# Performance work log

Hardware: AMD Instinct MI355X
Metric: run time of the kernel (lower is better)

## Reference

```python
import jax, jax.numpy as jnp
import numpy as np

NHEAD = 8
HEAD_DIM = 64
WIN = 16  # attention_window w


def _window_index(T, w):
    # For shift slot i in [0, 2w], window[i, t] corresponds to source index t + (i - w).
    W = 2 * w + 1
    j = jnp.arange(T)[None, :] + (jnp.arange(W) - w)[:, None]  # [W, T]
    valid = (j >= 0) & (j < T)
    return jnp.clip(j, 0, T - 1), valid


def setup_inputs() -> dict:
    key = jax.random.key(0)
    ks = jax.random.split(key, 8)
    B, T, N, E = 2, 256, 8, 512
    scale = 1.0 / np.sqrt(E).astype(np.float32)
    return {
        "query": jax.random.normal(ks[0], (B, T, N, E), jnp.float32),
        "key": jax.random.normal(ks[1], (B, T, N, E), jnp.float32),
        "value": jax.random.normal(ks[2], (B, T, N, E), jnp.float32),
        "key_padding_mask": jnp.zeros((B, T, N), dtype=bool),
        "Wq": jax.random.normal(ks[3], (E, E), jnp.float32) * scale,
        "bq": jnp.zeros((E,), jnp.float32),
        "Wk": jax.random.normal(ks[4], (E, E), jnp.float32) * scale,
        "bk": jnp.zeros((E,), jnp.float32),
        "Wv": jax.random.normal(ks[5], (E, E), jnp.float32) * scale,
        "bv": jnp.zeros((E,), jnp.float32),
    }


def reference(query, key, value, key_padding_mask, Wq, bq, Wk, bk, Wv, bv):
    B, T, N, E = query.shape
    h, d, w = NHEAD, HEAD_DIM, WIN
    W = 2 * w + 1
    # linear projections (torch nn.Linear: x @ W.T + b)
    q = (query @ Wq.T + bq).reshape(B, T, N, h, d) / np.float32(np.sqrt(d))
    k = (key @ Wk.T + bk).reshape(B, T, N, h, d)
    v = (value @ Wv.T + bv).reshape(B, T, N, h, d)

    jc, valid = _window_index(T, w)           # [W, T], [W, T]
    vmask6 = valid[None, :, :, None, None, None]
    kwin = jnp.where(vmask6, k[:, jc], 0.0)   # [B, W, T, N, h, d]
    vwin = jnp.where(vmask6, v[:, jc], 0.0)   # [B, W, T, N, h, d]
    # mask: True = masked out (out-of-range stays True, like generate_mask)
    mwin = jnp.where(valid[None, :, :, None], key_padding_mask[:, jc], True)  # [B, W, T, N]

    logits = jnp.einsum('btnhd,bwtmhd->btnwmh', q, kwin)  # [B,T,N,W,N,h]
    mask = mwin.transpose(0, 2, 1, 3)[:, :, None, :, :, None]  # [B,T,1,W,N,1]
    logits = jnp.where(mask, -jnp.inf, logits)

    attn = jax.nn.softmax(logits.reshape(B, T, N, W * N, h), axis=-2)

    vw = vwin.transpose(0, 2, 1, 3, 4, 5).reshape(B, T, W * N, h, d)
    out = jnp.einsum('btnmh,btmhd->btnhd', attn, vw).reshape(B, T, N, E)
    return out, attn
```

## Files before the change

### kernel.cpp

```cpp
#include <hip/hip_runtime.h>
#include <hip/hip_bf16.h>

#define TSEQ 256
#define NBATCH 2
#define NAG 8
#define NH 8
#define HD 64
#define EE 512
#define WHALF 16
#define WW 33
#define WN 264

typedef __attribute__((ext_vector_type(8))) short short8;
typedef __attribute__((ext_vector_type(4))) short short4v;
typedef __attribute__((ext_vector_type(4))) float f32x4;
typedef _Float16 f16x8 __attribute__((ext_vector_type(8)));

static __device__ __forceinline__ unsigned short f2bf(float f) {
    unsigned int u = __float_as_uint(f);
    unsigned int r = (u + 0x7FFFu + ((u >> 16) & 1u)) >> 16;
    return (unsigned short)r;
}
static __device__ __forceinline__ unsigned int cvt_pk_bf16(float lo, float hi) {
    unsigned int r;
    asm("v_cvt_pk_bf16_f32 %0, %1, %2" : "=v"(r) : "v"(lo), "v"(hi));
    return r;
}
static __device__ __forceinline__ unsigned short f2h(float f) {
    _Float16 h = (_Float16)f;
    return __builtin_bit_cast(unsigned short, h);
}
static __device__ __forceinline__ float h2f(unsigned short u) {
    return (float)__builtin_bit_cast(_Float16, u);
}
static __device__ __forceinline__ f16x8 as_f16x8(short8 s) {
    return __builtin_bit_cast(f16x8, s);
}

__global__ __launch_bounds__(256)
void proj_mfma_kernel(const float* __restrict__ xq, const float* __restrict__ xk,
                      const float* __restrict__ xv,
                      const float* __restrict__ Wq, const float* __restrict__ Wk,
                      const float* __restrict__ Wv,
                      const float* __restrict__ bq, const float* __restrict__ bk,
                      const float* __restrict__ bv,
                      unsigned short* __restrict__ oq,
                      unsigned short* __restrict__ kswz,
                      unsigned short* __restrict__ vswz)
{
    __shared__ __align__(16) char LS[24576];
    char* As = LS;
    char* Bs = LS + 8192;

    const float* x; const float* W; const float* bias; float scale;
    const int z = blockIdx.z;
    if (z == 0)      { x = xq; W = Wq; bias = bq; scale = 0.125f; }
    else if (z == 1) { x = xk; W = Wk; bias = bk; scale = 1.0f; }
    else             { x = xv; W = Wv; bias = bv; scale = 1.0f; }

    const int tid  = threadIdx.x;
    const int lane = tid & 63;
    const int wid  = tid >> 6;
    const int i0 = blockIdx.x * 64;
    const int f0 = blockIdx.y * 128;
    const int wr = wid >> 1, wc = wid & 1;

    f32x4 acc[2][4];
    #pragma unroll
    for (int m = 0; m < 2; ++m)
        #pragma unroll
        for (int n = 0; n < 4; ++n)
            acc[m][n] = (f32x4){0.f, 0.f, 0.f, 0.f};

    for (int k0 = 0; k0 < EE; k0 += 64) {
        #pragma unroll
        for (int it = 0; it < 4; ++it) {
            const int tt  = tid + it * 256;
            const int row = tt >> 4, f4 = tt & 15;
            float4 v4 = *reinterpret_cast<const float4*>(x + (size_t)(i0 + row) * EE + k0 + f4 * 4);
            uint2 u;
            u.x = cvt_pk_bf16(v4.x, v4.y);
            u.y = cvt_pk_bf16(v4.z, v4.w);
            *(uint2*)(As + row * 128 + ((f4 * 8) ^ ((row & 7) << 4))) = u;
        }
        #pragma unroll
        for (int it = 0; it < 8; ++it) {
            const int tt  = tid + it * 256;
            const int row = tt >> 4, f4 = tt & 15;
            float4 v4 = *reinterpret_cast<const float4*>(W + (size_t)(f0 + row) * EE + k0 + f4 * 4);
            uint2 u;
            u.x = cvt_pk_bf16(v4.x, v4.y);
            u.y = cvt_pk_bf16(v4.z, v4.w);
            *(uint2*)(Bs + row * 128 + ((f4 * 8) ^ ((row & 7) << 4))) = u;
        }
        __syncthreads();

        #pragma unroll
        for (int ks = 0; ks < 2; ++ks) {
            short8 a[2], b[4];
            #pragma unroll
            for (int m = 0; m < 2; ++m) {
                const int row = wr * 32 + m * 16 + (lane & 15);
                a[m] = *(short8*)(As + row * 128 +
                                  ((ks * 64 + (lane >> 4) * 16) ^ ((row & 7) << 4)));
            }
            #pragma unroll
            for (int n = 0; n < 4; ++n) {
                const int row = wc * 64 + n * 16 + (lane & 15);
                b[n] = *(short8*)(Bs + row * 128 +
                                  ((ks * 64 + (lane >> 4) * 16) ^ ((row & 7) << 4)));
            }
            #pragma unroll
            for (int m = 0; m < 2; ++m)
                #pragma unroll
                for (int n = 0; n < 4; ++n)
                    acc[m][n] = __builtin_amdgcn_mfma_f32_16x16x32_bf16(a[m], b[n], acc[m][n], 0, 0, 0);
        }
        __syncthreads();
    }

    if (z == 0) {
        #pragma unroll
        for (int n = 0; n < 4; ++n) {
            const int col = f0 + wc * 64 + n * 16 + (lane & 15);
            const float bb = bias[col];
            #pragma unroll
            for (int m = 0; m < 2; ++m)
                #pragma unroll
                for (int rg = 0; rg < 4; ++rg) {
                    const int row = i0 + wr * 32 + m * 16 + (lane >> 4) * 4 + rg;
                    oq[(size_t)row * EE + col] = f2bf((acc[m][n][rg] + bb) * scale);
                }
        }
    } else if (z == 1) {
        unsigned short* ls16 = (unsigned short*)LS;
        const int b_ = i0 >> 11;
        const int c0 = i0 & 2047;
        const int h0 = f0 >> 6;
        #pragma unroll
        for (int n = 0; n < 4; ++n) {
            const int col = f0 + wc * 64 + n * 16 + (lane & 15);
            const int hl = (col >> 6) & 1;
            const int d  = col & 63;
            const float bb = bias[col];
            const int ib = (d >> 5) * 512 + ((d & 31) >> 3) * 128 + (d & 7);
            #pragma unroll
            for (int m = 0; m < 2; ++m) {
                #pragma unroll
                for (int rg = 0; rg < 4; ++rg) {
                    const int cl = wr * 32 + m * 16 + (lane >> 4) * 4 + rg;
                    ls16[(hl * 4 + (cl >> 4)) * 1024 + ib + (cl & 15) * 8] =
                        f2bf(acc[m][n][rg] + bb);
                }
            }
        }
        __syncthreads();
        #pragma unroll
        for (int it = 0; it < 4; ++it) {
            const int ci = tid + it * 256;
            const int hlfg = ci >> 7;
            const int hl = hlfg >> 2, fg = hlfg & 3;
            short8 v = *(short8*)(ls16 + ci * 8);
            *(short8*)(kswz + (size_t)(b_ * 8 + h0 + hl) * 131072 +
                       (size_t)((c0 >> 4) + fg) * 1024 + (ci & 127) * 8) = v;
        }
    } else {
        unsigned short* ls16 = (unsigned short*)LS;
        const int b_ = i0 >> 11;
        const int c0 = i0 & 2047;
        const int h0 = f0 >> 6;
        #pragma unroll
        for (int n = 0; n < 4; ++n) {
            const int col = f0 + wc * 64 + n * 16 + (lane & 15);
            const int hl = (col >> 6) & 1;
            const int d  = col & 63;
            const float bb = bias[col];
            const int ib = (d >> 4) * 512 + (d & 15) * 8;
            #pragma unroll
            for (int m = 0; m < 2; ++m) {
                #pragma unroll
                for (int rg = 0; rg < 4; ++rg) {
                    const int cl = wr * 32 + m * 16 + (lane >> 4) * 4 + rg;
                    ls16[(hl * 2 + (cl >> 5)) * 2048 + ib + ((cl >> 3) & 3) * 128 + (cl & 7)] =
                        f2h(acc[m][n][rg] + bb);
                }
            }
        }
        __syncthreads();
        #pragma unroll
        for (int it = 0; it < 4; ++it) {
            const int ci = tid + it * 256;
            const int hlch = ci >> 8;
            const int hl = hlch >> 1, ch = hlch & 1;
            short8 v = *(short8*)(ls16 + ci * 8);
            *(short8*)(vswz + (size_t)(b_ * 8 + h0 + hl) * 131072 +
                       (size_t)((c0 >> 5) + ch) * 2048 + (ci & 255) * 8) = v;
        }
    }
}

#define RSW  296
#define HS   2376
#define KM_OFF_B  (8 * HS * 2)
#define INV_OFF_B (KM_OFF_B + 288)
#define SMEM2_BYTES (INV_OFF_B + 256 + 32)

__global__ __launch_bounds__(512, 4)
void attn_fused_kernel(const unsigned short* __restrict__ qb,
                       const unsigned short* __restrict__ kswz,
                       const unsigned short* __restrict__ vswz,
                       const unsigned char* __restrict__ kpm,
                       float* __restrict__ out,
                       float* __restrict__ attn)
{
    extern __shared__ char smem[];
    unsigned short* P16 = (unsigned short*)smem;
    char*  km   = smem + KM_OFF_B;
    float* invs = (float*)(smem + INV_OFF_B);

    const int bid = blockIdx.x;
    const int lin = (bid & 7) * 64 + (bid >> 3);
    const int b   = lin >> 8;
    const int t   = lin & 255;
    const int jstart = (t - WHALF) & ~3;
    const int off8   = ((t - WHALF) - jstart) * 8;
    const int fgbase = jstart >> 1;
    const int kcbase = jstart >> 2;
    const int tid = threadIdx.x;
    const int lane = tid & 63;
    const int h    = tid >> 6;

    if (tid < 288) {
        const int j = jstart + (tid >> 3), m = tid & 7;
        const bool v = (j >= 0) && (j < TSEQ) && (j >= t - WHALF) && (j <= t + WHALF)
                       && (kpm[(b * TSEQ + j) * NAG + m] == 0);
        km[tid] = v ? 1 : 0;
    }

    {
        const int n = lane & 7;
        const unsigned short* qbase = qb + ((size_t)(b * TSEQ + t) * NAG + n) * EE + h * HD;
        short8 aq0 = *(const short8*)(qbase + (lane >> 4) * 8);
        short8 aq1 = *(const short8*)(qbase + 32 + (lane >> 4) * 8);
        const unsigned short* kbase = kswz + (size_t)(b * 8 + h) * 131072;
        unsigned short* Ph = P16 + h * HS;
        const int r0 = (lane >> 4) * 4;
        const int cl = lane & 15;

        auto kfrag = [&](int f, int half) -> const short8* {
            int fg = fgbase + f;
            fg = (fg < 0) ? 0 : ((fg > 127) ? 127 : fg);
            return (const short8*)(kbase + fg * 1024 + half * 512 + lane * 8);
        };
        auto proc = [&](int f, short8 a0, short8 a1) {
            f32x4 a = (f32x4){0.f, 0.f, 0.f, 0.f};
            a = __builtin_amdgcn_mfma_f32_16x16x32_bf16(aq0, a0, a, 0, 0, 0);
            a = __builtin_amdgcn_mfma_f32_16x16x32_bf16(aq1, a1, a, 0, 0, 0);
            if (r0 < 8) {
                #pragma unroll
                for (int rg = 0; rg < 4; ++rg)
                    Ph[(r0 + rg) * RSW + f * 16 + cl] = f2h(a[rg]);
            }
        };

        short8 A0[6], B0[6], A1[6], B1[6];
        #pragma unroll
        for (int f = 0; f < 6; ++f) { A0[f] = *kfrag(f, 0); B0[f] = *kfrag(f, 1); }
        __builtin_amdgcn_sched_barrier(0);
        #pragma unroll
        for (int f = 0; f < 6; ++f) { A1[f] = *kfrag(6 + f, 0); B1[f] = *kfrag(6 + f, 1); }
        __builtin_amdgcn_sched_barrier(0);
        #pragma unroll
        for (int f = 0; f < 6; ++f) proc(f, A0[f], B0[f]);
        __builtin_amdgcn_sched_barrier(0);
        #pragma unroll
        for (int f = 0; f < 6; ++f) { A0[f] = *kfrag(12 + f, 0); B0[f] = *kfrag(12 + f, 1); }
        __builtin_amdgcn_sched_barrier(0);
        #pragma unroll
        for (int f = 0; f < 6; ++f) proc(6 + f, A1[f], B1[f]);
        __builtin_amdgcn_sched_barrier(0);
        #pragma unroll
        for (int f = 0; f < 6; ++f) proc(12 + f, A0[f], B0[f]);
    }
    __syncthreads();

    {
        const int r = lane & 7, sub = lane >> 3;
        unsigned short* prow = P16 + h * HS + r * RSW;
        float mx = -INFINITY;
        #pragma unroll
        for (int i = 0; i < 36; ++i) {
            const int c = sub + 8 * i;
            if (km[c]) mx = fmaxf(mx, h2f(prow[c]));
        }
        mx = fmaxf(mx, __shfl_xor(mx, 8));
        mx = fmaxf(mx, __shfl_xor(mx, 16));
        mx = fmaxf(mx, __shfl_xor(mx, 32));
        float sum = 0.f;
        #pragma unroll
        for (int i = 0; i < 36; ++i) {
            const int c = sub + 8 * i;
            float p = 0.f;
            if (km[c]) p = __expf(h2f(prow[c]) - mx);
            prow[c] = f2h(p);
            sum += p;
        }
        sum += __shfl_xor(sum, 8);
        sum += __shfl_xor(sum, 16);
        sum += __shfl_xor(sum, 32);
        if (sub == 0) invs[h * 8 + r] = 1.f / sum;
    }
    __syncthreads();

    const unsigned short* vbase = vswz + (size_t)(b * 8 + h) * 131072;
    auto vfrag = [&](int ms, int df) -> const short8* {
        int kc = kcbase + ms;
        kc = (kc < 0) ? 0 : ((kc > 63) ? 63 : kc);
        return (const short8*)(vbase + kc * 2048 + df * 512 + lane * 8);
    };
    short8 V0[3][4], V1[3][4];
    #pragma unroll
    for (int ms = 0; ms < 3; ++ms)
        #pragma unroll
        for (int df = 0; df < 4; ++df) V0[ms][df] = *vfrag(ms, df);
    __builtin_amdgcn_sched_barrier(0);

    {
        float* abase = attn + (size_t)(b * TSEQ + t) * (NAG * WN * NH);
        #pragma unroll 3
        for (int q4 = tid; q4 < 4224; q4 += 512) {
            const int hh = q4 & 1;
            const int rw = q4 >> 1;
            const int n  = rw / WN;
            const int wm = rw - n * WN;
            const int h0 = hh * 4;
            const unsigned short* pp = P16 + h0 * HS + n * RSW + wm + off8;
            float4 v;
            v.x = h2f(pp[0])      * invs[(h0 + 0) * 8 + n];
            v.y = h2f(pp[HS])     * invs[(h0 + 1) * 8 + n];
            v.z = h2f(pp[2 * HS]) * invs[(h0 + 2) * 8 + n];
            v.w = h2f(pp[3 * HS]) * invs[(h0 + 3) * 8 + n];
            *(float4*)(abase + (size_t)q4 * 4) = v;
        }
    }
    __builtin_amdgcn_sched_barrier(0);

    {
        const unsigned short* arow = P16 + h * HS + (lane & 7) * RSW;
        f32x4 acc[4];
        #pragma unroll
        for (int df = 0; df < 4; ++df) acc[df] = (f32x4){0.f, 0.f, 0.f, 0.f};

        auto consume = [&](int ms, short8 vv[4]) {
            short8 afr = *(const short8*)(arow + ms * 32 + (lane >> 4) * 8);
            #pragma unroll
            for (int df = 0; df < 4; ++df)
                acc[df] = __builtin_amdgcn_mfma_f32_16x16x32_f16(
                    as_f16x8(afr), as_f16x8(vv[df]), acc[df], 0, 0, 0);
        };

        #pragma unroll
        for (int ms = 0; ms < 3; ++ms)
            #pragma unroll
            for (int df = 0; df < 4; ++df) V1[ms][df] = *vfrag(3 + ms, df);
        __builtin_amdgcn_sched_barrier(0);
        #pragma unroll
        for (int ms = 0; ms < 3; ++ms) consume(ms, V0[ms]);
        __builtin_amdgcn_sched_barrier(0);
        #pragma unroll
        for (int ms = 0; ms < 3; ++ms)
            #pragma unroll
            for (int df = 0; df < 4; ++df) V0[ms][df] = *vfrag(6 + ms, df);
        __builtin_amdgcn_sched_barrier(0);
        #pragma unroll
        for (int ms = 0; ms < 3; ++ms) consume(3 + ms, V1[ms]);
        __builtin_amdgcn_sched_barrier(0);
        #pragma unroll
        for (int ms = 0; ms < 3; ++ms) consume(6 + ms, V0[ms]);

        const int r0 = (lane >> 4) * 4;
        if (r0 < 8) {
            float iv[4];
            #pragma unroll
            for (int rg = 0; rg < 4; ++rg) iv[rg] = invs[h * 8 + r0 + rg];
            #pragma unroll
            for (int df = 0; df < 4; ++df) {
                const int d = df * 16 + (lane & 15);
                #pragma unroll
                for (int rg = 0; rg < 4; ++rg) {
                    const int n = r0 + rg;
                    out[((size_t)(b * TSEQ + t) * NAG + n) * EE + h * HD + d] = acc[df][rg] * iv[rg];
                }
            }
        }
    }
}

extern "C" void kernel_launch(void* const* d_in, const int* in_sizes, int n_in,
                              void* d_out, int out_size, void* d_ws, size_t ws_size,
                              hipStream_t stream) {
    const float* query = (const float*)d_in[0];
    const float* key   = (const float*)d_in[1];
    const float* value = (const float*)d_in[2];
    const unsigned char* kpm = (const unsigned char*)d_in[3];
    const float* Wq = (const float*)d_in[4];
    const float* bq = (const float*)d_in[5];
    const float* Wk = (const float*)d_in[6];
    const float* bk = (const float*)d_in[7];
    const float* Wv = (const float*)d_in[8];
    const float* bv = (const float*)d_in[9];

    float* out  = (float*)d_out;
    float* attn = out + (size_t)NBATCH * TSEQ * NAG * EE;

    unsigned short* qbf  = (unsigned short*)d_ws;
    unsigned short* kswz = qbf + (size_t)4096 * EE;
    unsigned short* vswz = kswz + (size_t)4096 * EE;

    dim3 gp(64, 4, 3);
    proj_mfma_kernel<<<gp, 256, 0, stream>>>(query, key, value,
                                             Wq, Wk, Wv, bq, bk, bv,
                                             qbf, kswz, vswz);

    (void)hipFuncSetAttribute((const void*)attn_fused_kernel,
                              hipFuncAttributeMaxDynamicSharedMemorySize, SMEM2_BYTES);
    attn_fused_kernel<<<512, 512, SMEM2_BYTES, stream>>>(qbf, kswz, vswz, kpm, out, attn);
}
```

Baseline: 44.56 us.

## Process two query timesteps per block to fill all 16 MFMA rows

Each block now handles two consecutive timesteps, so the 16-row MFMA tiles carry 16 useful query rows instead of 8. That halves the grid and reuses each loaded K/V fragment for twice the work. The softmax now uses an additive half-precision mask with vectorized 8-wide LDS loads in place of per-element byte-mask branches. The costs are more shared memory per block, a lower occupancy hint in the launch bounds, and only 256 blocks in the grid.

```diff
diff --git a/kernel.cpp b/kernel.cpp
--- a/kernel.cpp
+++ b/kernel.cpp
@@ -200,12 +200,12 @@
 }
 
 #define RSW  296
-#define HS   2376
-#define KM_OFF_B  (8 * HS * 2)
-#define INV_OFF_B (KM_OFF_B + 288)
-#define SMEM2_BYTES (INV_OFF_B + 256 + 32)
-
-__global__ __launch_bounds__(512, 4)
+#define HS2  4744
+#define MV_OFF_B  (8 * HS2 * 2)
+#define INV_OFF_B (MV_OFF_B + 1152)
+#define SMEM2_BYTES (INV_OFF_B + 512 + 32)
+
+__global__ __launch_bounds__(512, 2)
 void attn_fused_kernel(const unsigned short* __restrict__ qb,
                        const unsigned short* __restrict__ kswz,
                        const unsigned short* __restrict__ vswz,
@@ -214,36 +214,42 @@
                        float* __restrict__ attn)
 {
     extern __shared__ char smem[];
-    unsigned short* P16 = (unsigned short*)smem;
-    char*  km   = smem + KM_OFF_B;
+    unsigned short* P16  = (unsigned short*)smem;
+    unsigned short* mv16 = (unsigned short*)(smem + MV_OFF_B);
     float* invs = (float*)(smem + INV_OFF_B);
 
     const int bid = blockIdx.x;
-    const int lin = (bid & 7) * 64 + (bid >> 3);
-    const int b   = lin >> 8;
-    const int t   = lin & 255;
-    const int jstart = (t - WHALF) & ~3;
-    const int off8   = ((t - WHALF) - jstart) * 8;
+    const int lin = (bid & 7) * 32 + (bid >> 3);
+    const int b   = lin >> 7;
+    const int tp  = lin & 127;
+    const int t0  = tp * 2;
+    const int jstart = (t0 - WHALF) & ~3;
+    const int off80  = ((t0 - WHALF) - jstart) * 8;
     const int fgbase = jstart >> 1;
     const int kcbase = jstart >> 2;
     const int tid = threadIdx.x;
     const int lane = tid & 63;
     const int h    = tid >> 6;
 
-    if (tid < 288) {
-        const int j = jstart + (tid >> 3), m = tid & 7;
-        const bool v = (j >= 0) && (j < TSEQ) && (j >= t - WHALF) && (j <= t + WHALF)
+    for (int i = tid; i < 576; i += 512) {
+        const int th = (i >= 288) ? 1 : 0;
+        const int c  = i - th * 288;
+        const int j  = jstart + (c >> 3), m = c & 7;
+        const int tt = t0 + th;
+        const bool v = (j >= 0) && (j < TSEQ) && (j >= tt - WHALF) && (j <= tt + WHALF)
                        && (kpm[(b * TSEQ + j) * NAG + m] == 0);
-        km[tid] = v ? 1 : 0;
-    }
+        mv16[i] = f2h(v ? 0.f : -30000.f);
+    }
+    __syncthreads();
 
     {
-        const int n = lane & 7;
-        const unsigned short* qbase = qb + ((size_t)(b * TSEQ + t) * NAG + n) * EE + h * HD;
+        const int row = lane & 15;
+        const int tq = t0 + (row >> 3), n = row & 7;
+        const unsigned short* qbase = qb + ((size_t)(b * TSEQ + tq) * NAG + n) * EE + h * HD;
         short8 aq0 = *(const short8*)(qbase + (lane >> 4) * 8);
         short8 aq1 = *(const short8*)(qbase + 32 + (lane >> 4) * 8);
         const unsigned short* kbase = kswz + (size_t)(b * 8 + h) * 131072;
-        unsigned short* Ph = P16 + h * HS;
+        unsigned short* Ph = P16 + h * HS2;
         const int r0 = (lane >> 4) * 4;
         const int cl = lane & 15;
 
@@ -256,11 +262,9 @@
             f32x4 a = (f32x4){0.f, 0.f, 0.f, 0.f};
             a = __builtin_amdgcn_mfma_f32_16x16x32_bf16(aq0, a0, a, 0, 0, 0);
             a = __builtin_amdgcn_mfma_f32_16x16x32_bf16(aq1, a1, a, 0, 0, 0);
-            if (r0 < 8) {
-                #pragma unroll
-                for (int rg = 0; rg < 4; ++rg)
-                    Ph[(r0 + rg) * RSW + f * 16 + cl] = f2h(a[rg]);
-            }
+            #pragma unroll
+            for (int rg = 0; rg < 4; ++rg)
+                Ph[(r0 + rg) * RSW + f * 16 + cl] = f2h(a[rg]);
         };
 
         short8 A0[6], B0[6], A1[6], B1[6];
@@ -285,30 +289,49 @@
     __syncthreads();
 
     {
-        const int r = lane & 7, sub = lane >> 3;
-        unsigned short* prow = P16 + h * HS + r * RSW;
+        const int r = lane & 15, sub = lane >> 4;
+        const int th = r >> 3;
+        unsigned short* prow = P16 + h * HS2 + r * RSW;
+        const unsigned short* mrow = mv16 + th * 288;
+        const int base = sub * 72;
+
+        short8 pv[9], mv[9];
+        #pragma unroll
+        for (int i = 0; i < 9; ++i) {
+            pv[i] = *(const short8*)(prow + base + i * 8);
+            mv[i] = *(const short8*)(mrow + base + i * 8);
+        }
         float mx = -INFINITY;
         #pragma unroll
-        for (int i = 0; i < 36; ++i) {
-            const int c = sub + 8 * i;
-            if (km[c]) mx = fmaxf(mx, h2f(prow[c]));
-        }
-        mx = fmaxf(mx, __shfl_xor(mx, 8));
+        for (int i = 0; i < 9; ++i)
+            #pragma unroll
+            for (int j = 0; j < 8; ++j) {
+                const float l = h2f((unsigned short)pv[i][j]) + h2f((unsigned short)mv[i][j]);
+                mx = fmaxf(mx, l);
+            }
         mx = fmaxf(mx, __shfl_xor(mx, 16));
         mx = fmaxf(mx, __shfl_xor(mx, 32));
+
         float sum = 0.f;
         #pragma unroll
-        for (int i = 0; i < 36; ++i) {
-            const int c = sub + 8 * i;
-            float p = 0.f;
-            if (km[c]) p = __expf(h2f(prow[c]) - mx);
-            prow[c] = f2h(p);
-            sum += p;
-        }
-        sum += __shfl_xor(sum, 8);
+        for (int i = 0; i < 9; ++i) {
+            float pj[8];
+            #pragma unroll
+            for (int j = 0; j < 8; ++j) {
+                const float l = h2f((unsigned short)pv[i][j]) + h2f((unsigned short)mv[i][j]);
+                pj[j] = __expf(l - mx);
+                sum += pj[j];
+            }
+            uint4 w;
+            w.x = (unsigned int)f2h(pj[0]) | ((unsigned int)f2h(pj[1]) << 16);
+            w.y = (unsigned int)f2h(pj[2]) | ((unsigned int)f2h(pj[3]) << 16);
+            w.z = (unsigned int)f2h(pj[4]) | ((unsigned int)f2h(pj[5]) << 16);
+            w.w = (unsigned int)f2h(pj[6]) | ((unsigned int)f2h(pj[7]) << 16);
+            *(uint4*)(prow + base + i * 8) = w;
+        }
         sum += __shfl_xor(sum, 16);
         sum += __shfl_xor(sum, 32);
-        if (sub == 0) invs[h * 8 + r] = 1.f / sum;
+        if (sub == 0) invs[h * 16 + r] = 1.f / sum;
     }
     __syncthreads();
 
@@ -326,27 +349,30 @@
     __builtin_amdgcn_sched_barrier(0);
 
     {
-        float* abase = attn + (size_t)(b * TSEQ + t) * (NAG * WN * NH);
-        #pragma unroll 3
-        for (int q4 = tid; q4 < 4224; q4 += 512) {
-            const int hh = q4 & 1;
-            const int rw = q4 >> 1;
-            const int n  = rw / WN;
-            const int wm = rw - n * WN;
-            const int h0 = hh * 4;
-            const unsigned short* pp = P16 + h0 * HS + n * RSW + wm + off8;
+        float* abase = attn + (size_t)(b * TSEQ + t0) * (NAG * WN * NH);
+        for (int q4 = tid; q4 < 8448; q4 += 512) {
+            const int hh  = q4 & 1;
+            const int rw  = q4 >> 1;
+            const int th  = (rw >= 2112) ? 1 : 0;
+            const int rem = rw - th * 2112;
+            const int n   = rem / WN;
+            const int wm  = rem - n * WN;
+            const int h0  = hh * 4;
+            const int col = wm + off80 + th * 8;
+            const unsigned short* pp = P16 + h0 * HS2 + (th * 8 + n) * RSW + col;
+            const int ivb = (th * 8 + n);
             float4 v;
-            v.x = h2f(pp[0])      * invs[(h0 + 0) * 8 + n];
-            v.y = h2f(pp[HS])     * invs[(h0 + 1) * 8 + n];
-            v.z = h2f(pp[2 * HS]) * invs[(h0 + 2) * 8 + n];
-            v.w = h2f(pp[3 * HS]) * invs[(h0 + 3) * 8 + n];
+            v.x = h2f(pp[0])       * invs[(h0 + 0) * 16 + ivb];
+            v.y = h2f(pp[HS2])     * invs[(h0 + 1) * 16 + ivb];
+            v.z = h2f(pp[2 * HS2]) * invs[(h0 + 2) * 16 + ivb];
+            v.w = h2f(pp[3 * HS2]) * invs[(h0 + 3) * 16 + ivb];
             *(float4*)(abase + (size_t)q4 * 4) = v;
         }
     }
     __builtin_amdgcn_sched_barrier(0);
 
     {
-        const unsigned short* arow = P16 + h * HS + (lane & 7) * RSW;
+        const unsigned short* arow = P16 + h * HS2 + (lane & 15) * RSW;
         f32x4 acc[4];
         #pragma unroll
         for (int df = 0; df < 4; ++df) acc[df] = (f32x4){0.f, 0.f, 0.f, 0.f};
@@ -379,18 +405,17 @@
         for (int ms = 0; ms < 3; ++ms) consume(6 + ms, V0[ms]);
 
         const int r0 = (lane >> 4) * 4;
-        if (r0 < 8) {
-            float iv[4];
-            #pragma unroll
-            for (int rg = 0; rg < 4; ++rg) iv[rg] = invs[h * 8 + r0 + rg];
-            #pragma unroll
-            for (int df = 0; df < 4; ++df) {
-                const int d = df * 16 + (lane & 15);
-                #pragma unroll
-                for (int rg = 0; rg < 4; ++rg) {
-                    const int n = r0 + rg;
-                    out[((size_t)(b * TSEQ + t) * NAG + n) * EE + h * HD + d] = acc[df][rg] * iv[rg];
-                }
+        float iv[4];
+        #pragma unroll
+        for (int rg = 0; rg < 4; ++rg) iv[rg] = invs[h * 16 + r0 + rg];
+        #pragma unroll
+        for (int df = 0; df < 4; ++df) {
+            const int d = df * 16 + (lane & 15);
+            #pragma unroll
+            for (int rg = 0; rg < 4; ++rg) {
+                const int row = r0 + rg;
+                const int t = t0 + (row >> 3), n = row & 7;
+                out[((size_t)(b * TSEQ + t) * NAG + n) * EE + h * HD + d] = acc[df][rg] * iv[rg];
             }
         }
     }
@@ -424,5 +449,5 @@
 
     (void)hipFuncSetAttribute((const void*)attn_fused_kernel,
                               hipFuncAttributeMaxDynamicSharedMemorySize, SMEM2_BYTES);
-    attn_fused_kernel<<<512, 512, SMEM2_BYTES, stream>>>(qbf, kswz, vswz, kpm, out, attn);
-}
+    attn_fused_kernel<<<256, 512, SMEM2_BYTES, stream>>>(qbf, kswz, vswz, kpm, out, attn);
+}
```

New measurement: 47.27 us. 6.1% more time.
